# Kernel optimization log

Hardware: AMD Instinct MI355X
Metric: run time of the kernel (lower is better)

The kernel has to match this reference:

```python
import jax, jax.numpy as jnp
import numpy as np

RES = (128, 128)       # frequency modes (fx, fy)
T = (1.0, 1.0)         # period per dimension
J = 2                  # simplex dimension (polygon)
B = 2                  # batch size
NV = 512               # num vertices = num elements (polygon ring)


def setup_inputs() -> dict:
    key = jax.random.key(0)
    V = jax.random.uniform(key, (B, NV, 2), dtype=jnp.float32)
    idx = jnp.arange(NV, dtype=jnp.int32)
    # polygon ring connectivity: edge i = (i, i+1 mod NV)
    E = jnp.broadcast_to(jnp.stack([idx, (idx + 1) % NV], axis=-1)[None], (B, NV, 2))
    D = jnp.ones((B, NV, 1), jnp.float32)
    return {"V": V, "E": E, "D": D}


def _omega():
    # freq_init='fft': integer fft/rfft frequencies, scaled by 2*pi/t per dim
    f0 = np.fft.fftfreq(RES[0], d=1.0 / RES[0])
    f1 = np.fft.rfftfreq(RES[1], d=1.0 / RES[1])
    om = np.stack(np.meshgrid(f0, f1, indexing='ij'), axis=-1).astype(np.float32)
    om[..., 0] *= 2.0 * np.pi / T[0]
    om[..., 1] *= 2.0 * np.pi / T[1]
    return jnp.asarray(om)  # (fx, fy//2+1, 2)


def reference(V, E, D):
    b, nv, nd = V.shape
    # subdim: append auxiliary origin vertex, turn edges into triangles
    Vaux = jnp.concatenate([V, jnp.zeros((b, 1, nd), V.dtype)], axis=1)
    Eaux = jnp.concatenate([E, jnp.full((b, E.shape[1], 1), nv, E.dtype)], axis=-1)
    P = jax.vmap(lambda v, e: v[e])(Vaux, Eaux)           # (B, ne, j+1, 2)
    # C = j! * signed simplex content = det of edge vectors (2x2)
    Vs = P[:, :, :J, :] - P[:, :, J:J + 1, :]
    C = (Vs[:, :, 0, 0] * Vs[:, :, 1, 1] - Vs[:, :, 0, 1] * Vs[:, :, 1, 0])[..., None]  # (B, ne, 1)
    omega = _omega()
    sig = jnp.einsum('bejd,xyd->bejxy', P, omega)         # (B, ne, 3, fx, fy2)
    esig = jnp.stack([jnp.cos(sig), -jnp.sin(sig)], axis=-1)  # (B, ne, 3, fx, fy2, 2)
    # divided-difference denominator: prod over circular shifts 1..j
    d1 = sig - sig[:, :, jnp.array([1, 2, 0])]
    d2 = sig - sig[:, :, jnp.array([2, 0, 1])]
    denom = d1 * d2
    zero = denom == 0
    tmp = jnp.sum(esig / jnp.where(zero, 1.0, denom)[..., None], axis=2)  # (B, ne, fx, fy2, 2)
    tmp = jnp.where(jnp.any(zero, axis=2)[..., None], 0.0, tmp)
    CD = C * D                                            # (B, ne, nch=1)
    F = jnp.einsum('bexyr,bec->bxycr', tmp, CD)           # (B, fx, fy2, 1, 2)
    # DC component: -1/j! * sum(C*D)
    dc = -jnp.sum(CD, axis=1) / 2.0                       # (B, 1)
    F = F.at[:, 0, 0].set(dc[..., None])
    F = -F                                                # img(F, deg=j=2): multiply by i^2 = -1
    F = F * (RES[0] ** J)                                 # density-preserving normalization
    return F
```

## Files before the change

### kernel.cpp

```cpp
#include <hip/hip_runtime.h>
#include <math.h>


#define NVERT 512
#define RESX  128
#define RESY2 65
#define BATCH 2
#define ESPLIT 2
#define CHUNKS 4

__device__ __forceinline__ float sig_eval(float x, float omx, float y, float omy) {
#pragma clang fp contract(off)
  float p = x * omx;
  float q = y * omy;
  return p + q;
}

extern "C" __global__ __launch_bounds__(512, 2)
void ddsl_spec(const float* __restrict__ V, const float* __restrict__ D,
               float* __restrict__ out) {
  const int kx = threadIdx.x;
  const int c  = threadIdx.y;
  const int ky = blockIdx.x;
  const int b  = blockIdx.y;
  const int z  = blockIdx.z;

  __shared__ float sVx[NVERT];
  __shared__ float sVy[NVERT];
  __shared__ float sCD[NVERT];
  __shared__ float red[2][CHUNKS][RESX];

  const int tid = threadIdx.y * RESX + threadIdx.x;

  {
    const float* Vb = V + b * (NVERT * 2);
    const int i = tid;
    const int j = (i + 1) & (NVERT - 1);
    float x0 = Vb[2 * i], y0 = Vb[2 * i + 1];
    float x1 = Vb[2 * j], y1 = Vb[2 * j + 1];
    float dv = D[b * NVERT + i];
    sVx[i] = x0;
    sVy[i] = y0;
    sCD[i] = (x0 * y1 - y0 * x1) * dv;
  }
  __syncthreads();

  const int   kxi = (kx < 64) ? kx : kx - 128;
  const float kxf = (float)kxi;
  const float kyf = (float)ky;
  const float TWO_PI = 6.2831854820251465f;
  const float omx = TWO_PI * kxf;
  const float omy = TWO_PI * kyf;

  const int e0 = (z * CHUNKS + c) * (NVERT / (ESPLIT * CHUNKS));
  const int elen = NVERT / (ESPLIT * CHUNKS);

  float x = sVx[e0], y = sVy[e0];
  float s0 = sig_eval(x, omx, y, omy);
  float r0 = kxf * x + kyf * y;
  float rf0 = __builtin_amdgcn_fractf(r0);
  float c0  = __builtin_amdgcn_cosf(rf0);
  float sn0 = __builtin_amdgcn_sinf(rf0);

  float accRe = 0.0f, accIm = 0.0f;

#pragma unroll 4
  for (int e = e0; e < e0 + elen; ++e) {
    const int j = (e + 1) & (NVERT - 1);
    float x1 = sVx[j], y1 = sVy[j];
    float cd = sCD[e];

    float s1 = sig_eval(x1, omx, y1, omy);
    float r1 = kxf * x1 + kyf * y1;
    float rf1 = __builtin_amdgcn_fractf(r1);
    float c1  = __builtin_amdgcn_cosf(rf1);
    float sn1 = __builtin_amdgcn_sinf(rf1);

    float d01 = s0 - s1;
    float prod = s0 * s1 * d01;
    bool invalid = (s0 == 0.0f) | (s1 == 0.0f) | (d01 == 0.0f) |
                   (fabsf(prod) < 1e-30f);
    float cdE = invalid ? 0.0f : cd;
    float pr  = invalid ? 1.0f : prod;
    float inv = __builtin_amdgcn_rcpf(pr);

    float a0 = s1 * inv;
    float a1 = s0 * inv;
    float a2 = d01 * inv;
    float re = fmaf(c0, a0, fmaf(-c1, a1, a2));
    float im = fmaf(sn1, a1, -(sn0 * a0));

    accRe = fmaf(cdE, re, accRe);
    accIm = fmaf(cdE, im, accIm);

    s0 = s1; c0 = c1; sn0 = sn1;
  }

  red[0][c][kx] = accRe;
  red[1][c][kx] = accIm;
  __syncthreads();

  if (c == 0) {
    float sRe = (red[0][0][kx] + red[0][1][kx]) + (red[0][2][kx] + red[0][3][kx]);
    float sIm = (red[1][0][kx] + red[1][1][kx]) + (red[1][2][kx] + red[1][3][kx]);
    float* o = out + b * (RESX * RESY2 * 2) + kx * (RESY2 * 2) + ky * 2;
    atomicAdd(o + 0, -16384.0f * sRe);
    atomicAdd(o + 1, -16384.0f * sIm);
  }

  if (ky == 0 && z == 0 && tid < 64) {
    float s = 0.0f;
#pragma unroll
    for (int k = tid; k < NVERT; k += 64) s += sCD[k];
    for (int off = 32; off > 0; off >>= 1) s += __shfl_down(s, off, 64);
    if (tid == 0) {
      float dc = 8192.0f * s;
      float* o = out + b * (RESX * RESY2 * 2);
      atomicAdd(o + 0, dc);
      atomicAdd(o + 1, dc);
    }
  }
}

extern "C" void kernel_launch(void* const* d_in, const int* in_sizes, int n_in,
                              void* d_out, int out_size, void* d_ws, size_t ws_size,
                              hipStream_t stream) {
  (void)in_sizes; (void)n_in; (void)d_ws; (void)ws_size;
  const float* V = (const float*)d_in[0];
  const float* D = (const float*)d_in[2];
  float* out = (float*)d_out;

  hipMemsetAsync(out, 0, (size_t)out_size * sizeof(float), stream);

  dim3 grid(RESY2, BATCH, ESPLIT);
  dim3 block(RESX, CHUNKS, 1);
  ddsl_spec<<<grid, block, 0, stream>>>(V, D, out);
}
```

Baseline: 71.89 us.

## Split kx across blocks so each block owns its outputs, dropping memset and atomics

Changes the work split from edge halves across blocks to kx halves across blocks, with 8 edge chunks per block reduced in shared memory. Each output is now written exactly once with a plain store, so the hipMemsetAsync and the atomicAdds go away. It also packs vertices as float2 in shared memory and reduces the invalid test to the single product magnitude check. In exchange each block now loops over all 512 edges with 64-wide kx rows, and the DC value goes through an extra barrier.

Result: faster. 68.77 us (-4.3%).

```diff
diff --git a/kernel.cpp b/kernel.cpp
--- a/kernel.cpp
+++ b/kernel.cpp
@@ -6,8 +6,9 @@
 #define RESX  128
 #define RESY2 65
 #define BATCH 2
-#define ESPLIT 2
-#define CHUNKS 4
+#define KXSPL 64
+#define CHUNKS 8
+#define ELEN  (NVERT / CHUNKS)
 
 __device__ __forceinline__ float sig_eval(float x, float omx, float y, float omy) {
 #pragma clang fp contract(off)
@@ -19,45 +20,44 @@
 extern "C" __global__ __launch_bounds__(512, 2)
 void ddsl_spec(const float* __restrict__ V, const float* __restrict__ D,
                float* __restrict__ out) {
-  const int kx = threadIdx.x;
-  const int c  = threadIdx.y;
-  const int ky = blockIdx.x;
-  const int b  = blockIdx.y;
-  const int z  = blockIdx.z;
+  const int lane = threadIdx.x;
+  const int c    = threadIdx.y;
+  const int ky   = blockIdx.x;
+  const int b    = blockIdx.y;
+  const int z    = blockIdx.z;
 
-  __shared__ float sVx[NVERT];
-  __shared__ float sVy[NVERT];
-  __shared__ float sCD[NVERT];
-  __shared__ float red[2][CHUNKS][RESX];
+  __shared__ float2 sV[NVERT];
+  __shared__ float  sCD[NVERT];
+  __shared__ float  red[2][CHUNKS][KXSPL];
+  __shared__ float  sDCv;
 
-  const int tid = threadIdx.y * RESX + threadIdx.x;
+  const int tid = c * KXSPL + lane;
 
   {
-    const float* Vb = V + b * (NVERT * 2);
+    const float2* Vb = (const float2*)(V + b * (NVERT * 2));
     const int i = tid;
     const int j = (i + 1) & (NVERT - 1);
-    float x0 = Vb[2 * i], y0 = Vb[2 * i + 1];
-    float x1 = Vb[2 * j], y1 = Vb[2 * j + 1];
+    float2 v0 = Vb[i];
+    float2 v1 = Vb[j];
     float dv = D[b * NVERT + i];
-    sVx[i] = x0;
-    sVy[i] = y0;
-    sCD[i] = (x0 * y1 - y0 * x1) * dv;
+    sV[i] = v0;
+    sCD[i] = (v0.x * v1.y - v0.y * v1.x) * dv;
   }
   __syncthreads();
 
-  const int   kxi = (kx < 64) ? kx : kx - 128;
+  const int kx = z * KXSPL + lane;
+  const int kxi = (kx < 64) ? kx : kx - 128;
   const float kxf = (float)kxi;
   const float kyf = (float)ky;
   const float TWO_PI = 6.2831854820251465f;
   const float omx = TWO_PI * kxf;
   const float omy = TWO_PI * kyf;
 
-  const int e0 = (z * CHUNKS + c) * (NVERT / (ESPLIT * CHUNKS));
-  const int elen = NVERT / (ESPLIT * CHUNKS);
+  const int e0 = c * ELEN;
 
-  float x = sVx[e0], y = sVy[e0];
-  float s0 = sig_eval(x, omx, y, omy);
-  float r0 = kxf * x + kyf * y;
+  float2 v = sV[e0];
+  float s0 = sig_eval(v.x, omx, v.y, omy);
+  float r0 = kxf * v.x + kyf * v.y;
   float rf0 = __builtin_amdgcn_fractf(r0);
   float c0  = __builtin_amdgcn_cosf(rf0);
   float sn0 = __builtin_amdgcn_sinf(rf0);
@@ -65,21 +65,20 @@
   float accRe = 0.0f, accIm = 0.0f;
 
 #pragma unroll 4
-  for (int e = e0; e < e0 + elen; ++e) {
+  for (int e = e0; e < e0 + ELEN; ++e) {
     const int j = (e + 1) & (NVERT - 1);
-    float x1 = sVx[j], y1 = sVy[j];
+    float2 v1 = sV[j];
     float cd = sCD[e];
 
-    float s1 = sig_eval(x1, omx, y1, omy);
-    float r1 = kxf * x1 + kyf * y1;
+    float s1 = sig_eval(v1.x, omx, v1.y, omy);
+    float r1 = kxf * v1.x + kyf * v1.y;
     float rf1 = __builtin_amdgcn_fractf(r1);
     float c1  = __builtin_amdgcn_cosf(rf1);
     float sn1 = __builtin_amdgcn_sinf(rf1);
 
     float d01 = s0 - s1;
     float prod = s0 * s1 * d01;
-    bool invalid = (s0 == 0.0f) | (s1 == 0.0f) | (d01 == 0.0f) |
-                   (fabsf(prod) < 1e-30f);
+    bool invalid = fabsf(prod) < 1e-30f;
     float cdE = invalid ? 0.0f : cd;
     float pr  = invalid ? 1.0f : prod;
     float inv = __builtin_amdgcn_rcpf(pr);
@@ -96,43 +95,40 @@
     s0 = s1; c0 = c1; sn0 = sn1;
   }
 
-  red[0][c][kx] = accRe;
-  red[1][c][kx] = accIm;
+  red[0][c][lane] = accRe;
+  red[1][c][lane] = accIm;
   __syncthreads();
 
-  if (c == 0) {
-    float sRe = (red[0][0][kx] + red[0][1][kx]) + (red[0][2][kx] + red[0][3][kx]);
-    float sIm = (red[1][0][kx] + red[1][1][kx]) + (red[1][2][kx] + red[1][3][kx]);
-    float* o = out + b * (RESX * RESY2 * 2) + kx * (RESY2 * 2) + ky * 2;
-    atomicAdd(o + 0, -16384.0f * sRe);
-    atomicAdd(o + 1, -16384.0f * sIm);
-  }
-
-  if (ky == 0 && z == 0 && tid < 64) {
+  float val = 0.0f;
+  if (c < 2) {
     float s = 0.0f;
 #pragma unroll
-    for (int k = tid; k < NVERT; k += 64) s += sCD[k];
+    for (int k = 0; k < CHUNKS; ++k) s += red[c][k][lane];
+    val = -16384.0f * s;
+  } else if (c == 2 && ky == 0 && z == 0) {
+    float s = 0.0f;
+#pragma unroll
+    for (int k = 0; k < NVERT / 64; ++k) s += sCD[lane + 64 * k];
     for (int off = 32; off > 0; off >>= 1) s += __shfl_down(s, off, 64);
-    if (tid == 0) {
-      float dc = 8192.0f * s;
-      float* o = out + b * (RESX * RESY2 * 2);
-      atomicAdd(o + 0, dc);
-      atomicAdd(o + 1, dc);
-    }
+    if (lane == 0) sDCv = 8192.0f * s;
+  }
+  __syncthreads();
+
+  if (c < 2) {
+    if (ky == 0 && z == 0 && lane == 0) val = sDCv;
+    out[b * (RESX * RESY2 * 2) + kx * (RESY2 * 2) + ky * 2 + c] = val;
   }
 }
 
 extern "C" void kernel_launch(void* const* d_in, const int* in_sizes, int n_in,
                               void* d_out, int out_size, void* d_ws, size_t ws_size,
                               hipStream_t stream) {
-  (void)in_sizes; (void)n_in; (void)d_ws; (void)ws_size;
+  (void)in_sizes; (void)n_in; (void)d_ws; (void)ws_size; (void)out_size;
   const float* V = (const float*)d_in[0];
   const float* D = (const float*)d_in[2];
   float* out = (float*)d_out;
 
-  hipMemsetAsync(out, 0, (size_t)out_size * sizeof(float), stream);
-
-  dim3 grid(RESY2, BATCH, ESPLIT);
-  dim3 block(RESX, CHUNKS, 1);
+  dim3 grid(RESY2, BATCH, 2);
+  dim3 block(KXSPL, CHUNKS, 1);
   ddsl_spec<<<grid, block, 0, stream>>>(V, D, out);
 }
```
